# Performance work log

Measured on AMD Instinct MI355X. Metric: run time of the kernel, lower is better.

Reference implementation:

```python
import jax, jax.numpy as jnp
import numpy as np

B, T, I, H = 32, 512, 512, 512  # batch, seq_len, input_size, hidden_size


def setup_inputs() -> dict:
    key = jax.random.key(0)
    ks = jax.random.split(key, 9)
    s = 1.0 / np.sqrt(H)  # PyTorch LSTM init: U(-1/sqrt(H), 1/sqrt(H))
    u = lambda k, shape: jax.random.uniform(k, shape, jnp.float32, -s, s)
    return {
        "x": jax.random.normal(ks[0], (B, T, I), jnp.float32),
        "h0": jnp.zeros((2, B, H), jnp.float32),
        "c0": jnp.zeros((2, B, H), jnp.float32),
        "w_ih_f": u(ks[1], (4 * H, I)), "w_hh_f": u(ks[2], (4 * H, H)),
        "b_ih_f": u(ks[3], (4 * H,)), "b_hh_f": u(ks[4], (4 * H,)),
        "w_ih_r": u(ks[5], (4 * H, I)), "w_hh_r": u(ks[6], (4 * H, H)),
        "b_ih_r": u(ks[7], (4 * H,)), "b_hh_r": u(ks[8], (4 * H,)),
    }


def _lstm_dir(x, h0, c0, w_ih, w_hh, b_ih, b_hh):
    # Precompute input projections for all timesteps: [T, B, 4H] (time-major for scan).
    gx = jnp.einsum('bti,gi->tbg', x, w_ih) + b_ih + b_hh

    def step(carry, g):
        h, c = carry
        g = g + h @ w_hh.T  # [B, 4H]
        i, f, gg, o = jnp.split(g, 4, axis=-1)  # PyTorch gate order: i, f, g, o
        c = jax.nn.sigmoid(f) * c + jax.nn.sigmoid(i) * jnp.tanh(gg)
        h = jax.nn.sigmoid(o) * jnp.tanh(c)
        return (h, c), h

    (hT, cT), hs = jax.lax.scan(step, (h0, c0), gx)
    return hs.transpose(1, 0, 2), hT, cT  # [B, T, H], [B, H], [B, H]


def reference(x, h0, c0, w_ih_f, w_hh_f, b_ih_f, b_hh_f,
              w_ih_r, w_hh_r, b_ih_r, b_hh_r):
    out_f, hT_f, cT_f = _lstm_dir(x, h0[0], c0[0], w_ih_f, w_hh_f, b_ih_f, b_hh_f)
    out_r, hT_r, cT_r = _lstm_dir(x[:, ::-1], h0[1], c0[1], w_ih_r, w_hh_r, b_ih_r, b_hh_r)
    out = jnp.concatenate([out_f, out_r[:, ::-1]], axis=-1)  # [B, T, 2H]
    h_n = jnp.stack([hT_f, hT_r])  # [2, B, H]
    c_n = jnp.stack([cT_f, cT_r])  # [2, B, H]
    return out, h_n, c_n
```

## Files before the change

### kernel.cpp

```cpp
#include <hip/hip_runtime.h>
#include <hip/hip_bf16.h>
#include <math.h>
#include <stdint.h>

#define BB 32
#define TT 512
#define II 512
#define HH 512
#define G4 (4 * HH)
#define MM (TT * BB)
#define BH (BB * HH)
#define WGD 32

typedef __hip_bfloat16 bf16;
typedef __attribute__((ext_vector_type(8))) short short8;
typedef __attribute__((ext_vector_type(4))) float f32x4;
typedef __attribute__((ext_vector_type(4))) unsigned u32x4;

__device__ __forceinline__ float bf2f(bf16 v) { return __bfloat162float(v); }
__device__ __forceinline__ bf16  f2bf(float v) { return __float2bfloat16(v); }
__device__ __forceinline__ short f2bs(float x) { bf16 v = f2bf(x); return *reinterpret_cast<short*>(&v); }
__device__ __forceinline__ float bs2f(short s) {
    unsigned u = ((unsigned)(unsigned short)s) << 16;
    return __uint_as_float(u);
}
__device__ __forceinline__ short8 pk8(float4 u, float4 v) {
    short8 t;
    t[0] = f2bs(u.x); t[1] = f2bs(u.y); t[2] = f2bs(u.z); t[3] = f2bs(u.w);
    t[4] = f2bs(v.x); t[5] = f2bs(v.y); t[6] = f2bs(v.z); t[7] = f2bs(v.w);
    return t;
}

#define GX1 ((size_t)TT * 4 * 128 * 128)

__global__ __launch_bounds__(256) void proj_mfma_kernel(
    const float* __restrict__ x,
    const float* __restrict__ w_f, const float* __restrict__ w_r,
    const float* __restrict__ bi_f, const float* __restrict__ bh_f,
    const float* __restrict__ bi_r, const float* __restrict__ bh_r,
    bf16* __restrict__ gx, int dir0)
{
    const int dl = blockIdx.z, dir = dir0 + dl;
    const int m0 = blockIdx.x * 64;
    const int n0 = blockIdx.y * 128;
    const float* __restrict__ w  = dir ? w_r  : w_f;
    const float* __restrict__ bi = dir ? bi_r : bi_f;
    const float* __restrict__ bh = dir ? bh_r : bh_f;

    __shared__ __align__(16) char smem[17408];
    bf16 (*As)[40]  = (bf16(*)[40])smem;
    bf16 (*Bs)[40]  = (bf16(*)[40])(smem + 5120);
    bf16 (*Cs)[136] = (bf16(*)[136])smem;

    const int tid = threadIdx.x;
    const int wv = tid >> 6, l = tid & 63;
    const int nl = l & 15, ko = (l >> 4) * 8;

    const int a_r = tid >> 2, a_s = tid & 3;
    const float* a_src = x + ((size_t)((m0 + a_r) & 31) * TT + (size_t)((m0 + a_r) >> 5)) * II + a_s * 8;
    const int b_r = tid >> 1, b_h = tid & 1;
    const float* b_src = w + (size_t)(n0 + b_r) * II + b_h * 16;

    f32x4 acc[8];
#pragma unroll
    for (int j = 0; j < 8; ++j) acc[j] = (f32x4){0.f, 0.f, 0.f, 0.f};

    float bias[8];
#pragma unroll
    for (int j = 0; j < 8; ++j) {
        const int n = n0 + j * 16 + nl;
        bias[j] = bi[n] + bh[n];
    }

    for (int k0 = 0; k0 < II; k0 += 32) {
        const float4 av0 = *(const float4*)(a_src + k0);
        const float4 av1 = *(const float4*)(a_src + k0 + 4);
        const float4 bv0 = *(const float4*)(b_src + k0);
        const float4 bv1 = *(const float4*)(b_src + k0 + 4);
        const float4 bv2 = *(const float4*)(b_src + k0 + 8);
        const float4 bv3 = *(const float4*)(b_src + k0 + 12);
        __syncthreads();
        *(short8*)&As[a_r][a_s * 8] = pk8(av0, av1);
        *(short8*)&Bs[b_r][b_h * 16]     = pk8(bv0, bv1);
        *(short8*)&Bs[b_r][b_h * 16 + 8] = pk8(bv2, bv3);
        __syncthreads();
        const short8 a = *(const short8*)&As[wv * 16 + nl][ko];
#pragma unroll
        for (int j = 0; j < 8; ++j) {
            const short8 b = *(const short8*)&Bs[j * 16 + nl][ko];
            acc[j] = __builtin_amdgcn_mfma_f32_16x16x32_bf16(a, b, acc[j], 0, 0, 0);
        }
    }

    __syncthreads();
    const int row0 = (l >> 4) * 4;
#pragma unroll
    for (int j = 0; j < 8; ++j)
#pragma unroll
        for (int r = 0; r < 4; ++r)
            Cs[wv * 16 + row0 + r][j * 16 + nl] = f2bf(acc[j][r] + bias[j]);
    __syncthreads();

    bf16* gxd = gx + (size_t)dl * GX1;
    const int g   = n0 >> 9;
    const int cgb = (n0 & 511) >> 2;
    const int t_base = blockIdx.x * 2;
#pragma unroll
    for (int i = 0; i < 4; ++i) {
        const int c = i * 256 + tid;
        const int tl = c >> 9, cgl = (c >> 4) & 31, u = c & 15;
        const int r0 = tl * 32 + 2 * u;
        const uint2 lo = *(const uint2*)&Cs[r0][cgl * 4];
        const uint2 hi = *(const uint2*)&Cs[r0 + 1][cgl * 4];
        uint4 ov; ov.x = lo.x; ov.y = lo.y; ov.z = hi.x; ov.w = hi.y;
        *(uint4*)(gxd + ((((size_t)(t_base + tl) * 4 + g) * 128 + cgb + cgl) * 128 + u * 8)) = ov;
    }
}

__device__ __forceinline__ void cell_step(
    const bf16 (*__restrict__ h_s)[520], const short8* __restrict__ bfrag,
    float (*__restrict__ exw)[36],
    const unsigned* __restrict__ gw,
    int nl, int ko, int l, int mC, int jjA,
    float& cs0, float& cs1, float& hv0, float& hv1)
{
    f32x4 acc0 = {0.f, 0.f, 0.f, 0.f};
    f32x4 acc1 = {0.f, 0.f, 0.f, 0.f};
#pragma unroll
    for (int half = 0; half < 2; ++half) {
        short8 a0[8], a1[8];
#pragma unroll
        for (int k = 0; k < 8; ++k) {
            const int ks = half * 8 + k;
            a0[k] = *(const short8*)&h_s[nl][ks * 32 + ko];
            a1[k] = *(const short8*)&h_s[nl + 16][ks * 32 + ko];
        }
#pragma unroll
        for (int k = 0; k < 8; ++k) {
            acc0 = __builtin_amdgcn_mfma_f32_16x16x32_bf16(a0[k], bfrag[half * 8 + k], acc0, 0, 0, 0);
            acc1 = __builtin_amdgcn_mfma_f32_16x16x32_bf16(a1[k], bfrag[half * 8 + k], acc1, 0, 0, 0);
        }
    }
    const int row0 = (l >> 4) * 4;
    *(f32x4*)&exw[nl][row0]      = acc0;
    *(f32x4*)&exw[nl][16 + row0] = acc1;

#pragma unroll
    for (int c = 0; c < 2; ++c) {
        const int jc = jjA + c;
        const int sh = 16 * c;
        float q0 = exw[0 * 4 + jc][mC] + bs2f((short)(gw[0] >> sh));
        float q1 = exw[1 * 4 + jc][mC] + bs2f((short)(gw[1] >> sh));
        float q2 = exw[2 * 4 + jc][mC] + bs2f((short)(gw[2] >> sh));
        float q3 = exw[3 * 4 + jc][mC] + bs2f((short)(gw[3] >> sh));
        q0 = fminf(fmaxf(q0, -30.f), 30.f);
        q1 = fminf(fmaxf(q1, -30.f), 30.f);
        q2 = fminf(fmaxf(q2, -30.f), 30.f);
        q3 = fminf(fmaxf(q3, -30.f), 30.f);
        const float ig = 1.f / (1.f + __expf(-q0));
        const float fg = 1.f / (1.f + __expf(-q1));
        const float te = __expf(2.f * q2);
        const float gg = (te - 1.f) / (te + 1.f);
        const float og = 1.f / (1.f + __expf(-q3));
        float cs = (c == 0) ? cs0 : cs1;
        cs = fg * cs + ig * gg;
        const float csc = fminf(fmaxf(cs, -15.f), 15.f);
        const float t2 = __expf(2.f * csc);
        const float th = (t2 - 1.f) / (t2 + 1.f);
        const float h = og * th;
        if (c == 0) { cs0 = cs; hv0 = h; } else { cs1 = cs; hv1 = h; }
    }
}

__global__ __launch_bounds__(256, 1) void lstm_rec_kernel(
    const bf16* __restrict__ gx,
    const float* __restrict__ h0, const float* __restrict__ c0,
    const float* __restrict__ whh_f, const float* __restrict__ whh_r,
    float* __restrict__ dout,
    bf16* __restrict__ h_buf,
    unsigned int* __restrict__ bars,
    int dir0)
{
    const int dl  = blockIdx.x >> 5;
    const int wgl = blockIdx.x & 31;
    const int dir = dir0 + dl;
    const int tid = threadIdx.x;
    const int wv  = tid >> 6;
    const int l   = tid & 63;
    const int cg  = wgl * 4 + wv;
    const int j0  = cg * 4;
    const float* __restrict__ whh = dir ? whh_r : whh_f;
    unsigned int* barsd = bars + (size_t)dl * 1024;

    __shared__ __align__(16) bf16 h_s[32][520];
    __shared__ __align__(16) float ex[4][16][36];

    const int nl = l & 15;
    const int g  = nl >> 2, jj = nl & 3;
    const int ko = (l >> 4) * 8;

    short8 bfrag[16];
    {
        const float* wr = whh + ((size_t)g * HH + (size_t)(j0 + jj)) * HH;
#pragma unroll
        for (int ks = 0; ks < 16; ++ks) {
            const float* p = wr + ks * 32 + ko;
            short8 t;
#pragma unroll
            for (int i = 0; i < 8; ++i) t[i] = f2bs(p[i]);
            bfrag[ks] = t;
        }
    }

    const int mC = l >> 1;
    const int jjA = (l & 1) * 2;

    float cs0, cs1;
    {
        const float* cp = c0 + (size_t)dir * BH + (size_t)mC * HH + j0 + jjA;
        cs0 = cp[0]; cs1 = cp[1];
    }

    bf16* hsl = h_buf + (size_t)dl * 2 * BH;
    const unsigned* gxw = (const unsigned*)(gx + (size_t)dl * GX1);

    for (int q = 0; q < 64; ++q) {
        const int f = q * 256 + tid;
        h_s[f >> 9][f & 511] = f2bf(h0[(size_t)dir * BH + f]);
    }
    __syncthreads();

    unsigned gw[4];
    {
        const int t0 = dir ? (TT - 1) : 0;
#pragma unroll
        for (int gg = 0; gg < 4; ++gg)
            gw[gg] = gxw[((size_t)(t0 * 4 + gg) * 128 + cg) * 64 + l];
    }

#pragma unroll 1
    for (int s = 0; s < TT; ++s) {
        const int t_x = dir ? (TT - 1 - s) : s;

        float hv0, hv1;
        cell_step(h_s, bfrag, ex[wv], gw, nl, ko, l, mC, jjA, cs0, cs1, hv0, hv1);

        if (s < TT - 1) {
            {
                bf16 hb0 = f2bf(hv0), hb1 = f2bf(hv1);
                unsigned pk = (unsigned)*(unsigned short*)&hb0 |
                              ((unsigned)*(unsigned short*)&hb1 << 16);
                unsigned* hp = (unsigned*)(hsl + (size_t)((s + 1) & 1) * BH + (size_t)mC * HH + j0 + jjA);
                __hip_atomic_store(hp, pk, __ATOMIC_RELAXED, __HIP_MEMORY_SCOPE_AGENT);
            }
            asm volatile("s_waitcnt vmcnt(0)" ::: "memory");
            __syncthreads();
            if (tid == 0)
                __hip_atomic_store(barsd + wgl * 32, (unsigned)(s + 1),
                                   __ATOMIC_RELAXED, __HIP_MEMORY_SCOPE_AGENT);

            {
                float2 ho; ho.x = hv0; ho.y = hv1;
                *(float2*)(dout + ((size_t)mC * TT + t_x) * (2 * HH) + (size_t)dir * HH + j0 + jjA) = ho;
            }
            const int t_n = dir ? (TT - 2 - s) : (s + 1);
            unsigned gwn[4];
#pragma unroll
            for (int gg = 0; gg < 4; ++gg)
                gwn[gg] = gxw[((size_t)(t_n * 4 + gg) * 128 + cg) * 64 + l];

            if (wv == 0) {
                const unsigned tgt = (unsigned)(s + 1);
                while (true) {
                    unsigned v = __hip_atomic_load(barsd + (l & 31) * 32,
                                                   __ATOMIC_RELAXED, __HIP_MEMORY_SCOPE_AGENT);
                    if (__all(v >= tgt)) break;
                    __builtin_amdgcn_s_sleep(1);
                }
            }
            __syncthreads();

            {
                const u32x4* src = (const u32x4*)(hsl + (size_t)((s + 1) & 1) * BH);
                u32x4 vv[8];
#pragma unroll
                for (int q = 0; q < 8; ++q) {
                    const u32x4* p = src + (q * 256 + tid);
                    asm volatile("global_load_dwordx4 %0, %1, off sc0 sc1"
                                 : "=v"(vv[q]) : "v"(p));
                }
                asm volatile("s_waitcnt vmcnt(0)" ::: "memory");
#pragma unroll
                for (int q = 0; q < 8; ++q) {
                    const int e = (q * 256 + tid) * 8;
                    *(u32x4*)&h_s[e >> 9][e & 511] = vv[q];
                }
            }
            __syncthreads();
#pragma unroll
            for (int gg = 0; gg < 4; ++gg) gw[gg] = gwn[gg];
        } else {
            float2 ho; ho.x = hv0; ho.y = hv1;
            *(float2*)(dout + ((size_t)mC * TT + t_x) * (2 * HH) + (size_t)dir * HH + j0 + jjA) = ho;
            const size_t hn_off = (size_t)BB * TT * 2 * HH;
            float2 co; co.x = cs0; co.y = cs1;
            *(float2*)(dout + hn_off + (size_t)dir * BH + (size_t)mC * HH + j0 + jjA) = ho;
            *(float2*)(dout + hn_off + 2 * (size_t)BH + (size_t)dir * BH + (size_t)mC * HH + j0 + jjA) = co;
        }
    }
}

extern "C" void kernel_launch(void* const* d_in, const int* in_sizes, int n_in,
                              void* d_out, int out_size, void* d_ws, size_t ws_size,
                              hipStream_t stream)
{
    (void)in_sizes; (void)n_in; (void)out_size;
    const float* x     = (const float*)d_in[0];
    const float* h0    = (const float*)d_in[1];
    const float* c0    = (const float*)d_in[2];
    const float* wih_f = (const float*)d_in[3];
    const float* whh_f = (const float*)d_in[4];
    const float* bih_f = (const float*)d_in[5];
    const float* bhh_f = (const float*)d_in[6];
    const float* wih_r = (const float*)d_in[7];
    const float* whh_r = (const float*)d_in[8];
    const float* bih_r = (const float*)d_in[9];
    const float* bhh_r = (const float*)d_in[10];
    float* out = (float*)d_out;

    const size_t gx1 = GX1 * sizeof(bf16);
    const size_t needA = 2 * gx1 + (size_t)4 * BH * sizeof(bf16) + 16384;
    char* ws = (char*)d_ws;

    if (ws_size >= needA) {
        bf16* gx = (bf16*)ws;
        bf16* h_buf = (bf16*)(ws + 2 * gx1);
        unsigned int* bars = (unsigned int*)(ws + 2 * gx1 + (size_t)4 * BH * sizeof(bf16));
        hipMemsetAsync(bars, 0, 8192, stream);
        dim3 g1(MM / 64, G4 / 128, 2);
        proj_mfma_kernel<<<g1, 256, 0, stream>>>(x, wih_f, wih_r, bih_f, bhh_f, bih_r, bhh_r, gx, 0);
        lstm_rec_kernel<<<dim3(2 * WGD), dim3(256), 0, stream>>>(
            gx, h0, c0, whh_f, whh_r, out, h_buf, bars, 0);
    } else {
        bf16* gx = (bf16*)ws;
        bf16* h_buf = (bf16*)(ws + gx1);
        unsigned int* bars = (unsigned int*)(ws + gx1 + (size_t)2 * BH * sizeof(bf16));
        for (int d = 0; d < 2; ++d) {
            hipMemsetAsync(bars, 0, 4096, stream);
            dim3 g1(MM / 64, G4 / 128, 1);
            proj_mfma_kernel<<<g1, 256, 0, stream>>>(x, wih_f, wih_r, bih_f, bhh_f, bih_r, bhh_r, gx, d);
            lstm_rec_kernel<<<dim3(WGD), dim3(256), 0, stream>>>(
                gx, h0, c0, whh_f, whh_r, out, h_buf, bars, d);
        }
    }
}
```

Before: 1.884 ms.

## Halve recurrent workgroups per direction, each wave computing two column groups

Cuts the persistent LSTM recurrence from 32 to 16 workgroups per direction, so each wave now holds W_hh fragments for two column groups and runs two cell steps per timestep. Fewer participants in the per-step global barrier should cut spin and synchronisation latency, and each workgroup reuses its staged h_s tile for twice the work. In exchange, the per-step compute on the critical path roughly doubles per wave and register pressure rises from holding two sets of bf16 weight fragments.

```diff
diff --git a/kernel.cpp b/kernel.cpp
--- a/kernel.cpp
+++ b/kernel.cpp
@@ -10,7 +10,7 @@
 #define G4 (4 * HH)
 #define MM (TT * BB)
 #define BH (BB * HH)
-#define WGD 32
+#define WGD 16
 
 typedef __hip_bfloat16 bf16;
 typedef __attribute__((ext_vector_type(8))) short short8;
@@ -181,44 +181,49 @@
     unsigned int* __restrict__ bars,
     int dir0)
 {
-    const int dl  = blockIdx.x >> 5;
-    const int wgl = blockIdx.x & 31;
+    const int dl  = blockIdx.x >> 4;
+    const int wgl = blockIdx.x & 15;
     const int dir = dir0 + dl;
     const int tid = threadIdx.x;
     const int wv  = tid >> 6;
     const int l   = tid & 63;
-    const int cg  = wgl * 4 + wv;
-    const int j0  = cg * 4;
+    const int cgA = wgl * 8 + wv * 2;
+    const int cgB = cgA + 1;
+    const int j0A = cgA * 4, j0B = cgB * 4;
     const float* __restrict__ whh = dir ? whh_r : whh_f;
-    unsigned int* barsd = bars + (size_t)dl * 1024;
+    unsigned int* barsd = bars + (size_t)dl * 512;
 
     __shared__ __align__(16) bf16 h_s[32][520];
-    __shared__ __align__(16) float ex[4][16][36];
+    __shared__ __align__(16) float ex[4][2][16][36];
 
     const int nl = l & 15;
     const int g  = nl >> 2, jj = nl & 3;
     const int ko = (l >> 4) * 8;
 
-    short8 bfrag[16];
+    short8 bfA[16], bfB[16];
     {
-        const float* wr = whh + ((size_t)g * HH + (size_t)(j0 + jj)) * HH;
+        const float* wrA = whh + ((size_t)g * HH + (size_t)(j0A + jj)) * HH;
+        const float* wrB = whh + ((size_t)g * HH + (size_t)(j0B + jj)) * HH;
 #pragma unroll
         for (int ks = 0; ks < 16; ++ks) {
-            const float* p = wr + ks * 32 + ko;
-            short8 t;
-#pragma unroll
-            for (int i = 0; i < 8; ++i) t[i] = f2bs(p[i]);
-            bfrag[ks] = t;
+            const float* pA = wrA + ks * 32 + ko;
+            const float* pB = wrB + ks * 32 + ko;
+            short8 tA, tB;
+#pragma unroll
+            for (int i = 0; i < 8; ++i) { tA[i] = f2bs(pA[i]); tB[i] = f2bs(pB[i]); }
+            bfA[ks] = tA; bfB[ks] = tB;
         }
     }
 
     const int mC = l >> 1;
     const int jjA = (l & 1) * 2;
 
-    float cs0, cs1;
+    float csA0, csA1, csB0, csB1;
     {
-        const float* cp = c0 + (size_t)dir * BH + (size_t)mC * HH + j0 + jjA;
-        cs0 = cp[0]; cs1 = cp[1];
+        const float* cpA = c0 + (size_t)dir * BH + (size_t)mC * HH + j0A + jjA;
+        const float* cpB = c0 + (size_t)dir * BH + (size_t)mC * HH + j0B + jjA;
+        csA0 = cpA[0]; csA1 = cpA[1];
+        csB0 = cpB[0]; csB1 = cpB[1];
     }
 
     bf16* hsl = h_buf + (size_t)dl * 2 * BH;
@@ -230,28 +235,37 @@
     }
     __syncthreads();
 
-    unsigned gw[4];
+    unsigned gwA[4], gwB[4];
     {
         const int t0 = dir ? (TT - 1) : 0;
 #pragma unroll
-        for (int gg = 0; gg < 4; ++gg)
-            gw[gg] = gxw[((size_t)(t0 * 4 + gg) * 128 + cg) * 64 + l];
+        for (int gg = 0; gg < 4; ++gg) {
+            gwA[gg] = gxw[((size_t)(t0 * 4 + gg) * 128 + cgA) * 64 + l];
+            gwB[gg] = gxw[((size_t)(t0 * 4 + gg) * 128 + cgB) * 64 + l];
+        }
     }
 
 #pragma unroll 1
     for (int s = 0; s < TT; ++s) {
         const int t_x = dir ? (TT - 1 - s) : s;
 
-        float hv0, hv1;
-        cell_step(h_s, bfrag, ex[wv], gw, nl, ko, l, mC, jjA, cs0, cs1, hv0, hv1);
+        float hvA0, hvA1, hvB0, hvB1;
+        cell_step(h_s, bfA, ex[wv][0], gwA, nl, ko, l, mC, jjA, csA0, csA1, hvA0, hvA1);
+        cell_step(h_s, bfB, ex[wv][1], gwB, nl, ko, l, mC, jjA, csB0, csB1, hvB0, hvB1);
 
         if (s < TT - 1) {
             {
-                bf16 hb0 = f2bf(hv0), hb1 = f2bf(hv1);
-                unsigned pk = (unsigned)*(unsigned short*)&hb0 |
-                              ((unsigned)*(unsigned short*)&hb1 << 16);
-                unsigned* hp = (unsigned*)(hsl + (size_t)((s + 1) & 1) * BH + (size_t)mC * HH + j0 + jjA);
-                __hip_atomic_store(hp, pk, __ATOMIC_RELAXED, __HIP_MEMORY_SCOPE_AGENT);
+                bf16 a0 = f2bf(hvA0), a1 = f2bf(hvA1);
+                bf16 b0 = f2bf(hvB0), b1 = f2bf(hvB1);
+                unsigned pkA = (unsigned)*(unsigned short*)&a0 |
+                               ((unsigned)*(unsigned short*)&a1 << 16);
+                unsigned pkB = (unsigned)*(unsigned short*)&b0 |
+                               ((unsigned)*(unsigned short*)&b1 << 16);
+                bf16* base = hsl + (size_t)((s + 1) & 1) * BH + (size_t)mC * HH;
+                __hip_atomic_store((unsigned*)(base + j0A + jjA), pkA,
+                                   __ATOMIC_RELAXED, __HIP_MEMORY_SCOPE_AGENT);
+                __hip_atomic_store((unsigned*)(base + j0B + jjA), pkB,
+                                   __ATOMIC_RELAXED, __HIP_MEMORY_SCOPE_AGENT);
             }
             asm volatile("s_waitcnt vmcnt(0)" ::: "memory");
             __syncthreads();
@@ -260,19 +274,24 @@
                                    __ATOMIC_RELAXED, __HIP_MEMORY_SCOPE_AGENT);
 
             {
-                float2 ho; ho.x = hv0; ho.y = hv1;
-                *(float2*)(dout + ((size_t)mC * TT + t_x) * (2 * HH) + (size_t)dir * HH + j0 + jjA) = ho;
+                float* db = dout + ((size_t)mC * TT + t_x) * (2 * HH) + (size_t)dir * HH;
+                float2 ha; ha.x = hvA0; ha.y = hvA1;
+                float2 hb; hb.x = hvB0; hb.y = hvB1;
+                *(float2*)(db + j0A + jjA) = ha;
+                *(float2*)(db + j0B + jjA) = hb;
             }
             const int t_n = dir ? (TT - 2 - s) : (s + 1);
-            unsigned gwn[4];
-#pragma unroll
-            for (int gg = 0; gg < 4; ++gg)
-                gwn[gg] = gxw[((size_t)(t_n * 4 + gg) * 128 + cg) * 64 + l];
+            unsigned gwnA[4], gwnB[4];
+#pragma unroll
+            for (int gg = 0; gg < 4; ++gg) {
+                gwnA[gg] = gxw[((size_t)(t_n * 4 + gg) * 128 + cgA) * 64 + l];
+                gwnB[gg] = gxw[((size_t)(t_n * 4 + gg) * 128 + cgB) * 64 + l];
+            }
 
             if (wv == 0) {
                 const unsigned tgt = (unsigned)(s + 1);
                 while (true) {
-                    unsigned v = __hip_atomic_load(barsd + (l & 31) * 32,
+                    unsigned v = __hip_atomic_load(barsd + (l & 15) * 32,
                                                    __ATOMIC_RELAXED, __HIP_MEMORY_SCOPE_AGENT);
                     if (__all(v >= tgt)) break;
                     __builtin_amdgcn_s_sleep(1);
@@ -298,14 +317,22 @@
             }
             __syncthreads();
 #pragma unroll
-            for (int gg = 0; gg < 4; ++gg) gw[gg] = gwn[gg];
+            for (int gg = 0; gg < 4; ++gg) { gwA[gg] = gwnA[gg]; gwB[gg] = gwnB[gg]; }
         } else {
-            float2 ho; ho.x = hv0; ho.y = hv1;
-            *(float2*)(dout + ((size_t)mC * TT + t_x) * (2 * HH) + (size_t)dir * HH + j0 + jjA) = ho;
             const size_t hn_off = (size_t)BB * TT * 2 * HH;
-            float2 co; co.x = cs0; co.y = cs1;
-            *(float2*)(dout + hn_off + (size_t)dir * BH + (size_t)mC * HH + j0 + jjA) = ho;
-            *(float2*)(dout + hn_off + 2 * (size_t)BH + (size_t)dir * BH + (size_t)mC * HH + j0 + jjA) = co;
+            float* db = dout + ((size_t)mC * TT + t_x) * (2 * HH) + (size_t)dir * HH;
+            float2 ha; ha.x = hvA0; ha.y = hvA1;
+            float2 hb; hb.x = hvB0; hb.y = hvB1;
+            *(float2*)(db + j0A + jjA) = ha;
+            *(float2*)(db + j0B + jjA) = hb;
+            float* hn = dout + hn_off + (size_t)dir * BH + (size_t)mC * HH;
+            float* cn = dout + hn_off + 2 * (size_t)BH + (size_t)dir * BH + (size_t)mC * HH;
+            *(float2*)(hn + j0A + jjA) = ha;
+            *(float2*)(hn + j0B + jjA) = hb;
+            float2 ca; ca.x = csA0; ca.y = csA1;
+            float2 cb; cb.x = csB0; cb.y = csB1;
+            *(float2*)(cn + j0A + jjA) = ca;
+            *(float2*)(cn + j0B + jjA) = cb;
         }
     }
 }
```

After: 2.525 ms. +34.1%, slower.
